# Performance work log

Hardware: AMD Instinct MI355X
Metric: run time of the kernel (lower is better)

Reference implementation:

```python
import jax, jax.numpy as jnp
import numpy as np

N, F, H, C, E = 100000, 128, 128, 40, 1600000


def setup_inputs() -> dict:
    key = jax.random.key(0)
    ks = jax.random.split(key, 8)
    x = jax.random.normal(ks[0], (N, F), dtype=jnp.float32)
    edge_index = jax.random.randint(ks[1], (2, E), 0, N, dtype=jnp.int64)
    s = 0.05
    return {
        "x": x,
        "edge_index": edge_index,
        "eps1": jnp.float32(0.0),
        "w1": jax.random.normal(ks[2], (F, H), dtype=jnp.float32) * s,
        "b1": jnp.zeros((H,), jnp.float32),
        "w2": jax.random.normal(ks[3], (H, H), dtype=jnp.float32) * s,
        "b2": jnp.zeros((H,), jnp.float32),
        "eps2": jnp.float32(0.0),
        "w3": jax.random.normal(ks[4], (H, H), dtype=jnp.float32) * s,
        "b3": jnp.zeros((H,), jnp.float32),
        "w4": jax.random.normal(ks[5], (H, C), dtype=jnp.float32) * s,
        "b4": jnp.zeros((C,), jnp.float32),
    }


def _gin_aggregate(h, src, dst, eps, n):
    # sum_{j -> i} h_j  +  (1+eps) * h_i
    agg = jax.ops.segment_sum(h[src], dst, num_segments=n)
    return (1.0 + eps) * h + agg


def reference(x, edge_index, eps1, w1, b1, w2, b2, eps2, w3, b3, w4, b4):
    src, dst = edge_index[0], edge_index[1]
    n = x.shape[0]
    # conv1: GINConv with MLP = Lin-ReLU-Lin-ReLU
    h = _gin_aggregate(x, src, dst, eps1, n)
    h = jax.nn.relu(h @ w1 + b1)
    h = jax.nn.relu(h @ w2 + b2)
    h = jax.nn.relu(h)  # outer F.relu (idempotent, kept for faithfulness)
    # dropout: identity in eval mode
    # conv2: GINConv with MLP = Lin-ReLU-Lin
    h2 = _gin_aggregate(h, src, dst, eps2, n)
    h2 = jax.nn.relu(h2 @ w3 + b3)
    h2 = h2 @ w4 + b4
    return jax.nn.log_softmax(h2, axis=1)
```

## Files before the change

kernel.cpp:

```cpp
#include <hip/hip_runtime.h>
#include <hip/hip_fp16.h>
#include <math.h>

constexpr int F = 128;
constexpr int C = 40;
constexpr int LDH = 136;
constexpr int BSHIFT = 8;
constexpr int BSIZE = 1 << BSHIFT;
constexpr int CHUNK = 8192;

typedef __attribute__((ext_vector_type(8))) _Float16 half8;
typedef __attribute__((ext_vector_type(4))) float float4v;


__global__ __launch_bounds__(256) void coarse_hist_kernel(const int* __restrict__ dst, int E, int NB,
                                                          int* __restrict__ coarse_count) {
    __shared__ int hist[512];
    int t = threadIdx.x;
    int c0 = blockIdx.x * CHUNK;
    int cend = min(c0 + CHUNK, E);
    for (int i = t; i < NB; i += 256) hist[i] = 0;
    __syncthreads();
    for (int i = c0 + t; i < cend; i += 256)
        atomicAdd(&hist[dst[i] >> BSHIFT], 1);
    __syncthreads();
    for (int i = t; i < NB; i += 256)
        if (hist[i]) atomicAdd(&coarse_count[i], hist[i]);
}

__global__ __launch_bounds__(512) void coarse_scan_kernel(const int* __restrict__ coarse_count,
                                                          int NB, int E,
                                                          int* __restrict__ coarse_start,
                                                          int* __restrict__ bucket_pos,
                                                          int* __restrict__ row_start, int N) {
    __shared__ int tmp[512];
    int t = threadIdx.x;
    int v = (t < NB) ? coarse_count[t] : 0;
    tmp[t] = v;
    __syncthreads();
    for (int d = 1; d < 512; d <<= 1) {
        int add = (t >= d) ? tmp[t - d] : 0;
        __syncthreads();
        tmp[t] += add;
        __syncthreads();
    }
    if (t < NB) {
        int ex = tmp[t] - v;
        coarse_start[t] = ex;
        bucket_pos[t] = ex;
    }
    if (t == 0) {
        coarse_start[NB] = E;
        row_start[N] = E;
    }
}

__global__ __launch_bounds__(256) void bucket_scatter_a_kernel(
        const int* __restrict__ src, const int* __restrict__ dst, int E, int NB,
        int* __restrict__ bucket_pos, unsigned* __restrict__ pairs) {
    __shared__ int hist[512];
    __shared__ int base[512];
    int t = threadIdx.x;
    int c0 = blockIdx.x * CHUNK;
    int cend = min(c0 + CHUNK, E);
    for (int i = t; i < NB; i += 256) hist[i] = 0;
    __syncthreads();
    for (int i = c0 + t; i < cend; i += 256)
        atomicAdd(&hist[dst[i] >> BSHIFT], 1);
    __syncthreads();
    for (int i = t; i < NB; i += 256) {
        int h = hist[i];
        base[i] = (h > 0) ? atomicAdd(&bucket_pos[i], h) : 0;
        hist[i] = 0;
    }
    __syncthreads();
    for (int i = c0 + t; i < cend; i += 256) {
        int d = dst[i];
        int b = d >> BSHIFT;
        int p = base[b] + atomicAdd(&hist[b], 1);
        pairs[p] = ((unsigned)(d & (BSIZE - 1)) << 24) | (unsigned)src[i];
    }
}

__global__ __launch_bounds__(256) void bucket_sort_kernel(const unsigned* __restrict__ pairs,
                                                          const int* __restrict__ coarse_start,
                                                          int N, int* __restrict__ row_start,
                                                          int* __restrict__ src_sorted) {
    __shared__ int hist[256];
    __shared__ int tmp[256];
    int b = blockIdx.x, t = threadIdx.x;
    int base = b << BSHIFT;
    int start = coarse_start[b];
    int end = coarse_start[b + 1];
    hist[t] = 0;
    __syncthreads();
    for (int i = start + t; i < end; i += 256)
        atomicAdd(&hist[pairs[i] >> 24], 1);
    __syncthreads();
    int v = hist[t];
    tmp[t] = v;
    __syncthreads();
    for (int d = 1; d < 256; d <<= 1) {
        int add = (t >= d) ? tmp[t - d] : 0;
        __syncthreads();
        tmp[t] += add;
        __syncthreads();
    }
    int ex = start + tmp[t] - v;
    if (base + t < N) row_start[base + t] = ex;
    hist[t] = ex;
    __syncthreads();
    for (int i = start + t; i < end; i += 256) {
        unsigned u = pairs[i];
        int p = atomicAdd(&hist[u >> 24], 1);
        src_sorted[p] = (int)(u & 0x00FFFFFFu);
    }
}


__global__ void conv_f16_kernel(const float* __restrict__ in, __half* __restrict__ out, int n4,
                                int* __restrict__ coarse_count, int NB) {
    int i = blockIdx.x * blockDim.x + threadIdx.x;
    if (blockIdx.x == 0) {
        for (int j = threadIdx.x; j < NB; j += 256) coarse_count[j] = 0;
    }
    if (i >= n4) return;
    float4 v = ((const float4*)in)[i];
    __half2 a = __floats2half2_rn(v.x, v.y);
    __half2 b = __floats2half2_rn(v.z, v.w);
    uint2 o;
    o.x = __builtin_bit_cast(unsigned, a);
    o.y = __builtin_bit_cast(unsigned, b);
    ((uint2*)out)[i] = o;
}


__global__ __launch_bounds__(256) void prep_weights_kernel(
        const float* __restrict__ w1, const float* __restrict__ w2,
        const float* __restrict__ w3, const float* __restrict__ w4,
        __half* __restrict__ w1t, __half* __restrict__ w2t,
        __half* __restrict__ w3t, __half* __restrict__ w4t) {
    __shared__ float lds[128 * 128];
    const float* in; __half* outp; int Nin, Npad;
    switch (blockIdx.x) {
        case 0:  in = w1; outp = w1t; Nin = 128; Npad = 128; break;
        case 1:  in = w2; outp = w2t; Nin = 128; Npad = 128; break;
        case 2:  in = w3; outp = w3t; Nin = 128; Npad = 128; break;
        default: in = w4; outp = w4t; Nin = 40;  Npad = 48;  break;
    }
    int t = threadIdx.x;
    int nf4 = 128 * Nin / 4;
    for (int i = t; i < nf4; i += 256)
        ((float4*)lds)[i] = ((const float4*)in)[i];
    __syncthreads();
    int total = Npad * 64;
    for (int i = t; i < total; i += 256) {
        int n = i >> 6, k2 = (i & 63) * 2;
        float lo = 0.f, hi = 0.f;
        if (n < Nin) {
            lo = lds[k2 * Nin + n];
            hi = lds[(k2 + 1) * Nin + n];
        }
        __half2 h = __floats2half2_rn(lo, hi);
        ((unsigned*)outp)[i] = __builtin_bit_cast(unsigned, h);
    }
}


__global__ __launch_bounds__(256) void agg_f16_kernel(const __half* __restrict__ feat,
        const int* __restrict__ row_start, const int* __restrict__ src_sorted,
        const float* __restrict__ eps_ptr, __half* __restrict__ out, int N) {
    int wid = (int)((blockIdx.x * blockDim.x + threadIdx.x) >> 6);
    int lane = threadIdx.x & 63;
    if (wid >= N) return;
    int q = lane >> 4, l16 = lane & 15;
    int s = row_start[wid], e = row_start[wid + 1];
    uint4 selfu = *(((const uint4*)(feat + (size_t)wid * F)) + l16);
    float ep1 = 1.0f + *eps_ptr;
    __half2 A0, A1, A2, A3, B0, B1, B2, B3;
    A0 = A1 = A2 = A3 = B0 = B1 = B2 = B3 = __builtin_bit_cast(__half2, 0u);
    const uint4 z4 = make_uint4(0u, 0u, 0u, 0u);
    for (int i0 = s; i0 < e; i0 += 16) {
        int li = i0 + l16;
        int sv = src_sorted[li < e ? li : (e - 1)];
        int s0 = __shfl(sv, q);
        int s1 = __shfl(sv, q + 4);
        int s2 = __shfl(sv, q + 8);
        int s3 = __shfl(sv, q + 12);
        uint4 u0 = *(((const uint4*)(feat + (size_t)s0 * F)) + l16);
        uint4 u1 = *(((const uint4*)(feat + (size_t)s1 * F)) + l16);
        uint4 u2 = *(((const uint4*)(feat + (size_t)s2 * F)) + l16);
        uint4 u3 = *(((const uint4*)(feat + (size_t)s3 * F)) + l16);
        if (i0 + q >= e)      u0 = z4;
        if (i0 + q + 4 >= e)  u1 = z4;
        if (i0 + q + 8 >= e)  u2 = z4;
        if (i0 + q + 12 >= e) u3 = z4;
        A0 = __hadd2(A0, __builtin_bit_cast(__half2, u0.x));
        A1 = __hadd2(A1, __builtin_bit_cast(__half2, u0.y));
        A2 = __hadd2(A2, __builtin_bit_cast(__half2, u0.z));
        A3 = __hadd2(A3, __builtin_bit_cast(__half2, u0.w));
        B0 = __hadd2(B0, __builtin_bit_cast(__half2, u1.x));
        B1 = __hadd2(B1, __builtin_bit_cast(__half2, u1.y));
        B2 = __hadd2(B2, __builtin_bit_cast(__half2, u1.z));
        B3 = __hadd2(B3, __builtin_bit_cast(__half2, u1.w));
        A0 = __hadd2(A0, __builtin_bit_cast(__half2, u2.x));
        A1 = __hadd2(A1, __builtin_bit_cast(__half2, u2.y));
        A2 = __hadd2(A2, __builtin_bit_cast(__half2, u2.z));
        A3 = __hadd2(A3, __builtin_bit_cast(__half2, u2.w));
        B0 = __hadd2(B0, __builtin_bit_cast(__half2, u3.x));
        B1 = __hadd2(B1, __builtin_bit_cast(__half2, u3.y));
        B2 = __hadd2(B2, __builtin_bit_cast(__half2, u3.z));
        B3 = __hadd2(B3, __builtin_bit_cast(__half2, u3.w));
    }
    float a[8];
    {
        float2 fa, fb;
        fa = __half22float2(A0); fb = __half22float2(B0); a[0] = fa.x + fb.x; a[1] = fa.y + fb.y;
        fa = __half22float2(A1); fb = __half22float2(B1); a[2] = fa.x + fb.x; a[3] = fa.y + fb.y;
        fa = __half22float2(A2); fb = __half22float2(B2); a[4] = fa.x + fb.x; a[5] = fa.y + fb.y;
        fa = __half22float2(A3); fb = __half22float2(B3); a[6] = fa.x + fb.x; a[7] = fa.y + fb.y;
    }
#pragma unroll
    for (int j = 0; j < 8; ++j) {
        a[j] += __shfl_xor(a[j], 16);
        a[j] += __shfl_xor(a[j], 32);
    }
    if (q == 0) {
        float2 s0 = __half22float2(__builtin_bit_cast(__half2, selfu.x));
        float2 s1 = __half22float2(__builtin_bit_cast(__half2, selfu.y));
        float2 s2 = __half22float2(__builtin_bit_cast(__half2, selfu.z));
        float2 s3 = __half22float2(__builtin_bit_cast(__half2, selfu.w));
        a[0] = fmaf(ep1, s0.x, a[0]); a[1] = fmaf(ep1, s0.y, a[1]);
        a[2] = fmaf(ep1, s1.x, a[2]); a[3] = fmaf(ep1, s1.y, a[3]);
        a[4] = fmaf(ep1, s2.x, a[4]); a[5] = fmaf(ep1, s2.y, a[5]);
        a[6] = fmaf(ep1, s3.x, a[6]); a[7] = fmaf(ep1, s3.y, a[7]);
        uint4 ou;
        ou.x = __builtin_bit_cast(unsigned, __floats2half2_rn(a[0], a[1]));
        ou.y = __builtin_bit_cast(unsigned, __floats2half2_rn(a[2], a[3]));
        ou.z = __builtin_bit_cast(unsigned, __floats2half2_rn(a[4], a[5]));
        ou.w = __builtin_bit_cast(unsigned, __floats2half2_rn(a[6], a[7]));
        *(((uint4*)(out + (size_t)wid * F)) + l16) = ou;
    }
}


__global__ __launch_bounds__(256) void mlp1_mfma_kernel(const __half* __restrict__ A,
        const __half* __restrict__ w1t, const float* __restrict__ b1,
        const __half* __restrict__ w2t, const float* __restrict__ b2,
        __half* __restrict__ out, int N) {
    __shared__ __half ldsA[64 * LDH];
    __shared__ __half ldsW[128 * LDH];
    __shared__ float ldsB[256];
    int t = threadIdx.x;
    int wave = t >> 6, lane = t & 63, quad = lane >> 4, l16 = lane & 15;
    int br = blockIdx.x * 64;
    if (t < 128) ldsB[t] = b1[t];
    else         ldsB[t] = b2[t - 128];
    for (int i = t; i < 1024; i += 256) {
        int r = i >> 4, c = i & 15;
        int gr = br + r;
        uint4 v = make_uint4(0u, 0u, 0u, 0u);
        if (gr < N) v = *((const uint4*)(A + (size_t)gr * F + c * 8));
        *((uint4*)&ldsA[r * LDH + c * 8]) = v;
    }
    for (int i = t; i < 2048; i += 256) {
        int r = i >> 4, c = i & 15;
        *((uint4*)&ldsW[r * LDH + c * 8]) = *((const uint4*)(w1t + r * 128 + c * 8));
    }
    __syncthreads();

    int ct0 = wave * 2;
    float4v acc[4][2];
    float4v zero = {0.f, 0.f, 0.f, 0.f};
#pragma unroll
    for (int i = 0; i < 4; ++i)
#pragma unroll
        for (int j = 0; j < 2; ++j) acc[i][j] = zero;

#pragma unroll
    for (int ks = 0; ks < 4; ++ks) {
        half8 af[4], wf[2];
#pragma unroll
        for (int i = 0; i < 4; ++i)
            af[i] = *((const half8*)&ldsA[(i * 16 + l16) * LDH + ks * 32 + quad * 8]);
#pragma unroll
        for (int j = 0; j < 2; ++j)
            wf[j] = *((const half8*)&ldsW[((ct0 + j) * 16 + l16) * LDH + ks * 32 + quad * 8]);
#pragma unroll
        for (int i = 0; i < 4; ++i)
#pragma unroll
            for (int j = 0; j < 2; ++j)
                acc[i][j] = __builtin_amdgcn_mfma_f32_16x16x32_f16(wf[j], af[i], acc[i][j], 0, 0, 0);
    }
    __syncthreads();
#pragma unroll
    for (int j = 0; j < 2; ++j) {
        int c = ct0 + j;
        float4 bb = *((const float4*)&ldsB[c * 16 + quad * 4]);
#pragma unroll
        for (int i = 0; i < 4; ++i) {
            float v0 = acc[i][j][0] + bb.x; v0 = v0 > 0.f ? v0 : 0.f;
            float v1 = acc[i][j][1] + bb.y; v1 = v1 > 0.f ? v1 : 0.f;
            float v2 = acc[i][j][2] + bb.z; v2 = v2 > 0.f ? v2 : 0.f;
            float v3 = acc[i][j][3] + bb.w; v3 = v3 > 0.f ? v3 : 0.f;
            __half2 h0 = __floats2half2_rn(v0, v1);
            __half2 h1 = __floats2half2_rn(v2, v3);
            uint2 o;
            o.x = __builtin_bit_cast(unsigned, h0);
            o.y = __builtin_bit_cast(unsigned, h1);
            *((uint2*)&ldsA[(i * 16 + l16) * LDH + c * 16 + quad * 4]) = o;
        }
    }
    for (int i = t; i < 2048; i += 256) {
        int r = i >> 4, c = i & 15;
        *((uint4*)&ldsW[r * LDH + c * 8]) = *((const uint4*)(w2t + r * 128 + c * 8));
    }
    __syncthreads();

#pragma unroll
    for (int i = 0; i < 4; ++i)
#pragma unroll
        for (int j = 0; j < 2; ++j) acc[i][j] = zero;
#pragma unroll
    for (int ks = 0; ks < 4; ++ks) {
        half8 af[4], wf[2];
#pragma unroll
        for (int i = 0; i < 4; ++i)
            af[i] = *((const half8*)&ldsA[(i * 16 + l16) * LDH + ks * 32 + quad * 8]);
#pragma unroll
        for (int j = 0; j < 2; ++j)
            wf[j] = *((const half8*)&ldsW[((ct0 + j) * 16 + l16) * LDH + ks * 32 + quad * 8]);
#pragma unroll
        for (int i = 0; i < 4; ++i)
#pragma unroll
            for (int j = 0; j < 2; ++j)
                acc[i][j] = __builtin_amdgcn_mfma_f32_16x16x32_f16(wf[j], af[i], acc[i][j], 0, 0, 0);
    }
    __syncthreads();
#pragma unroll
    for (int j = 0; j < 2; ++j) {
        int c = ct0 + j;
        float4 bb = *((const float4*)&ldsB[128 + c * 16 + quad * 4]);
#pragma unroll
        for (int i = 0; i < 4; ++i) {
            float v0 = acc[i][j][0] + bb.x; v0 = v0 > 0.f ? v0 : 0.f;
            float v1 = acc[i][j][1] + bb.y; v1 = v1 > 0.f ? v1 : 0.f;
            float v2 = acc[i][j][2] + bb.z; v2 = v2 > 0.f ? v2 : 0.f;
            float v3 = acc[i][j][3] + bb.w; v3 = v3 > 0.f ? v3 : 0.f;
            __half2 h0 = __floats2half2_rn(v0, v1);
            __half2 h1 = __floats2half2_rn(v2, v3);
            uint2 o;
            o.x = __builtin_bit_cast(unsigned, h0);
            o.y = __builtin_bit_cast(unsigned, h1);
            *((uint2*)&ldsA[(i * 16 + l16) * LDH + c * 16 + quad * 4]) = o;
        }
    }
    __syncthreads();
    for (int i = t; i < 1024; i += 256) {
        int r = i >> 4, c = i & 15;
        int gr = br + r;
        if (gr < N)
            *((uint4*)(out + (size_t)gr * F + c * 8)) = *((const uint4*)&ldsA[r * LDH + c * 8]);
    }
}


__global__ __launch_bounds__(256) void mlp2_mfma_kernel(const __half* __restrict__ A,
        const __half* __restrict__ w3t, const float* __restrict__ b3,
        const __half* __restrict__ w4t, const float* __restrict__ b4,
        float* __restrict__ out, int N) {
    __shared__ __half ldsA[64 * LDH];
    __shared__ __half ldsW[128 * LDH];
    __shared__ float ldsB[176];
    int t = threadIdx.x;
    int wave = t >> 6, lane = t & 63, quad = lane >> 4, l16 = lane & 15;
    int br = blockIdx.x * 64;
    if (t < 128) ldsB[t] = b3[t];
    else if (t < 176) ldsB[t] = (t - 128 < C) ? b4[t - 128] : 0.f;
    for (int i = t; i < 1024; i += 256) {
        int r = i >> 4, c = i & 15;
        int gr = br + r;
        uint4 v = make_uint4(0u, 0u, 0u, 0u);
        if (gr < N) v = *((const uint4*)(A + (size_t)gr * F + c * 8));
        *((uint4*)&ldsA[r * LDH + c * 8]) = v;
    }
    for (int i = t; i < 2048; i += 256) {
        int r = i >> 4, c = i & 15;
        *((uint4*)&ldsW[r * LDH + c * 8]) = *((const uint4*)(w3t + r * 128 + c * 8));
    }
    __syncthreads();

    int ct0 = wave * 2;
    float4v acc[4][2];
    float4v zero = {0.f, 0.f, 0.f, 0.f};
#pragma unroll
    for (int i = 0; i < 4; ++i)
#pragma unroll
        for (int j = 0; j < 2; ++j) acc[i][j] = zero;
#pragma unroll
    for (int ks = 0; ks < 4; ++ks) {
        half8 af[4], wf[2];
#pragma unroll
        for (int i = 0; i < 4; ++i)
            af[i] = *((const half8*)&ldsA[(i * 16 + l16) * LDH + ks * 32 + quad * 8]);
#pragma unroll
        for (int j = 0; j < 2; ++j)
            wf[j] = *((const half8*)&ldsW[((ct0 + j) * 16 + l16) * LDH + ks * 32 + quad * 8]);
#pragma unroll
        for (int i = 0; i < 4; ++i)
#pragma unroll
            for (int j = 0; j < 2; ++j)
                acc[i][j] = __builtin_amdgcn_mfma_f32_16x16x32_f16(wf[j], af[i], acc[i][j], 0, 0, 0);
    }
    __syncthreads();
#pragma unroll
    for (int j = 0; j < 2; ++j) {
        int c = ct0 + j;
        float4 bb = *((const float4*)&ldsB[c * 16 + quad * 4]);
#pragma unroll
        for (int i = 0; i < 4; ++i) {
            float v0 = acc[i][j][0] + bb.x; v0 = v0 > 0.f ? v0 : 0.f;
            float v1 = acc[i][j][1] + bb.y; v1 = v1 > 0.f ? v1 : 0.f;
            float v2 = acc[i][j][2] + bb.z; v2 = v2 > 0.f ? v2 : 0.f;
            float v3 = acc[i][j][3] + bb.w; v3 = v3 > 0.f ? v3 : 0.f;
            __half2 h0 = __floats2half2_rn(v0, v1);
            __half2 h1 = __floats2half2_rn(v2, v3);
            uint2 o;
            o.x = __builtin_bit_cast(unsigned, h0);
            o.y = __builtin_bit_cast(unsigned, h1);
            *((uint2*)&ldsA[(i * 16 + l16) * LDH + c * 16 + quad * 4]) = o;
        }
    }
    for (int i = t; i < 768; i += 256) {
        int r = i >> 4, c = i & 15;
        *((uint4*)&ldsW[r * LDH + c * 8]) = *((const uint4*)(w4t + r * 128 + c * 8));
    }
    __syncthreads();

    float4v acc4[3];
#pragma unroll
    for (int c = 0; c < 3; ++c) acc4[c] = zero;
#pragma unroll
    for (int ks = 0; ks < 4; ++ks) {
        half8 af = *((const half8*)&ldsA[(wave * 16 + l16) * LDH + ks * 32 + quad * 8]);
#pragma unroll
        for (int c = 0; c < 3; ++c) {
            half8 wf = *((const half8*)&ldsW[(c * 16 + l16) * LDH + ks * 32 + quad * 8]);
            acc4[c] = __builtin_amdgcn_mfma_f32_16x16x32_f16(wf, af, acc4[c], 0, 0, 0);
        }
    }
    float lv[3][4];
#pragma unroll
    for (int c = 0; c < 3; ++c) {
        float4 bb = *((const float4*)&ldsB[128 + c * 16 + quad * 4]);
        lv[c][0] = acc4[c][0] + bb.x;
        lv[c][1] = acc4[c][1] + bb.y;
        lv[c][2] = acc4[c][2] + bb.z;
        lv[c][3] = acc4[c][3] + bb.w;
    }
    bool tile2ok = (quad < 2);
    float m = -1e30f;
#pragma unroll
    for (int c = 0; c < 3; ++c) {
        if (c == 2 && !tile2ok) continue;
#pragma unroll
        for (int r = 0; r < 4; ++r) m = fmaxf(m, lv[c][r]);
    }
    m = fmaxf(m, __shfl_xor(m, 16));
    m = fmaxf(m, __shfl_xor(m, 32));
    float ssum = 0.f;
#pragma unroll
    for (int c = 0; c < 3; ++c) {
        if (c == 2 && !tile2ok) continue;
#pragma unroll
        for (int r = 0; r < 4; ++r) ssum += __expf(lv[c][r] - m);
    }
    ssum += __shfl_xor(ssum, 16);
    ssum += __shfl_xor(ssum, 32);
    float L = m + __logf(ssum);
    int node = br + wave * 16 + l16;
    if (node < N) {
#pragma unroll
        for (int c = 0; c < 3; ++c) {
            if (c == 2 && !tile2ok) continue;
            float4 o = make_float4(lv[c][0] - L, lv[c][1] - L, lv[c][2] - L, lv[c][3] - L);
            *((float4*)(out + (size_t)node * C + c * 16 + quad * 4)) = o;
        }
    }
}


extern "C" void kernel_launch(void* const* d_in, const int* in_sizes, int n_in,
                              void* d_out, int out_size, void* d_ws, size_t ws_size,
                              hipStream_t stream) {
    const float* x    = (const float*)d_in[0];
    const int*   ei   = (const int*)d_in[1];
    const float* eps1 = (const float*)d_in[2];
    const float* w1   = (const float*)d_in[3];
    const float* b1   = (const float*)d_in[4];
    const float* w2   = (const float*)d_in[5];
    const float* b2   = (const float*)d_in[6];
    const float* eps2 = (const float*)d_in[7];
    const float* w3   = (const float*)d_in[8];
    const float* b3   = (const float*)d_in[9];
    const float* w4   = (const float*)d_in[10];
    const float* b4   = (const float*)d_in[11];
    float* out = (float*)d_out;

    int N = in_sizes[0] / F;
    int E = in_sizes[1] / 2;
    const int* src = ei;
    const int* dst = ei + E;

    int NB = (N + BSIZE - 1) >> BSHIFT;
    int BA = (E + CHUNK - 1) / CHUNK;

    __half* x_h  = (__half*)d_ws;
    __half* h0_h = x_h + (size_t)N * F;
    __half* h_h  = h0_h + (size_t)N * F;
    __half* w1t  = h_h + (size_t)N * F;
    __half* w2t  = w1t + 128 * 128;
    __half* w3t  = w2t + 128 * 128;
    __half* w4t  = w3t + 128 * 128;
    unsigned* pairs   = (unsigned*)(w4t + 48 * 128);
    int* row_start    = (int*)(pairs + E);
    int* src_sorted   = row_start + (N + 1);
    int* coarse_count = src_sorted + E;
    int* coarse_start = coarse_count + 512;
    int* bucket_pos   = coarse_start + 513;

    int n4 = N * F / 4;
    conv_f16_kernel<<<(n4 + 255) / 256, 256, 0, stream>>>(x, x_h, n4, coarse_count, NB);
    prep_weights_kernel<<<4, 256, 0, stream>>>(w1, w2, w3, w4, w1t, w2t, w3t, w4t);

    coarse_hist_kernel<<<BA, 256, 0, stream>>>(dst, E, NB, coarse_count);
    coarse_scan_kernel<<<1, 512, 0, stream>>>(coarse_count, NB, E, coarse_start, bucket_pos,
                                              row_start, N);
    bucket_scatter_a_kernel<<<BA, 256, 0, stream>>>(src, dst, E, NB, bucket_pos, pairs);
    bucket_sort_kernel<<<NB, 256, 0, stream>>>(pairs, coarse_start, N, row_start, src_sorted);

    agg_f16_kernel<<<(N + 3) / 4, 256, 0, stream>>>(x_h, row_start, src_sorted, eps1, h0_h, N);
    mlp1_mfma_kernel<<<(N + 63) / 64, 256, 0, stream>>>(h0_h, w1t, b1, w2t, b2, h_h, N);
    agg_f16_kernel<<<(N + 3) / 4, 256, 0, stream>>>(h_h, row_start, src_sorted, eps2, h0_h, N);
    mlp2_mfma_kernel<<<(N + 63) / 64, 256, 0, stream>>>(h0_h, w3t, b3, w4t, b4, out, N);
}
```

Measured before the change: 346.0 us.

## Fuse neighbor aggregation into MFMA MLP kernels and merge prep kernels

Neighbor aggregation is fused into each MLP kernel: every wave aggregates 16 rows straight into LDS, then the MFMA layers run on that tile, so the intermediate aggregated feature buffer is never written to or read from global memory. Weight fragments are now read directly from global memory (cached) instead of being staged in LDS, which shrinks LDS use. The histogram, weight transpose and x conversion are merged into one launch, with a memset replacing the in-kernel zeroing. The trade-off is less aggregation parallelism per block (64 rows handled serially by 4 waves) and more repeated global weight loads.

```diff
diff --git a/kernel.cpp b/kernel.cpp
--- a/kernel.cpp
+++ b/kernel.cpp
@@ -13,20 +13,64 @@
 typedef __attribute__((ext_vector_type(4))) float float4v;
 
 
-__global__ __launch_bounds__(256) void coarse_hist_kernel(const int* __restrict__ dst, int E, int NB,
-                                                          int* __restrict__ coarse_count) {
-    __shared__ int hist[512];
-    int t = threadIdx.x;
-    int c0 = blockIdx.x * CHUNK;
-    int cend = min(c0 + CHUNK, E);
-    for (int i = t; i < NB; i += 256) hist[i] = 0;
-    __syncthreads();
-    for (int i = c0 + t; i < cend; i += 256)
-        atomicAdd(&hist[dst[i] >> BSHIFT], 1);
-    __syncthreads();
-    for (int i = t; i < NB; i += 256)
-        if (hist[i]) atomicAdd(&coarse_count[i], hist[i]);
-}
+__global__ __launch_bounds__(256) void fused_prep_kernel(
+        const float* __restrict__ x, __half* __restrict__ x_h, int n4,
+        const int* __restrict__ dst, int E, int NB, int* __restrict__ coarse_count,
+        const float* __restrict__ w1, const float* __restrict__ w2,
+        const float* __restrict__ w3, const float* __restrict__ w4,
+        __half* __restrict__ w1t, __half* __restrict__ w2t,
+        __half* __restrict__ w3t, __half* __restrict__ w4t, int BA) {
+    __shared__ float smem[4096];
+    int b = blockIdx.x, t = threadIdx.x;
+    if (b < BA) {
+        int* hist = (int*)smem;
+        int c0 = b * CHUNK, cend = min(c0 + CHUNK, E);
+        for (int i = t; i < NB; i += 256) hist[i] = 0;
+        __syncthreads();
+        for (int i = c0 + t; i < cend; i += 256)
+            atomicAdd(&hist[dst[i] >> BSHIFT], 1);
+        __syncthreads();
+        for (int i = t; i < NB; i += 256)
+            if (hist[i]) atomicAdd(&coarse_count[i], hist[i]);
+        return;
+    }
+    if (b < BA + 4) {
+        const float* in; __half* outp; int Nin, Npad;
+        switch (b - BA) {
+            case 0:  in = w1; outp = w1t; Nin = 128; Npad = 128; break;
+            case 1:  in = w2; outp = w2t; Nin = 128; Npad = 128; break;
+            case 2:  in = w3; outp = w3t; Nin = 128; Npad = 128; break;
+            default: in = w4; outp = w4t; Nin = 40;  Npad = 48;  break;
+        }
+        for (int p = 0; p < 4; ++p) {
+            int nf4 = 32 * Nin / 4;
+            const float4* srcv = (const float4*)(in + 32 * p * Nin);
+            for (int i = t; i < nf4; i += 256) ((float4*)smem)[i] = srcv[i];
+            __syncthreads();
+            int total = Npad * 16;
+            for (int i = t; i < total; i += 256) {
+                int n = i >> 4, wl = i & 15;
+                float lo = 0.f, hi = 0.f;
+                if (n < Nin) {
+                    lo = smem[(2 * wl) * Nin + n];
+                    hi = smem[(2 * wl + 1) * Nin + n];
+                }
+                __half2 h = __floats2half2_rn(lo, hi);
+                ((unsigned*)outp)[n * 64 + 16 * p + wl] = __builtin_bit_cast(unsigned, h);
+            }
+            __syncthreads();
+        }
+        return;
+    }
+    int i = (b - BA - 4) * 256 + t;
+    if (i >= n4) return;
+    float4 v = ((const float4*)x)[i];
+    uint2 o;
+    o.x = __builtin_bit_cast(unsigned, __floats2half2_rn(v.x, v.y));
+    o.y = __builtin_bit_cast(unsigned, __floats2half2_rn(v.z, v.w));
+    ((uint2*)x_h)[i] = o;
+}
+
 
 __global__ __launch_bounds__(512) void coarse_scan_kernel(const int* __restrict__ coarse_count,
                                                           int NB, int E,
@@ -118,154 +162,94 @@
 }
 
 
-__global__ void conv_f16_kernel(const float* __restrict__ in, __half* __restrict__ out, int n4,
-                                int* __restrict__ coarse_count, int NB) {
-    int i = blockIdx.x * blockDim.x + threadIdx.x;
-    if (blockIdx.x == 0) {
-        for (int j = threadIdx.x; j < NB; j += 256) coarse_count[j] = 0;
-    }
-    if (i >= n4) return;
-    float4 v = ((const float4*)in)[i];
-    __half2 a = __floats2half2_rn(v.x, v.y);
-    __half2 b = __floats2half2_rn(v.z, v.w);
-    uint2 o;
-    o.x = __builtin_bit_cast(unsigned, a);
-    o.y = __builtin_bit_cast(unsigned, b);
-    ((uint2*)out)[i] = o;
-}
-
-
-__global__ __launch_bounds__(256) void prep_weights_kernel(
-        const float* __restrict__ w1, const float* __restrict__ w2,
-        const float* __restrict__ w3, const float* __restrict__ w4,
-        __half* __restrict__ w1t, __half* __restrict__ w2t,
-        __half* __restrict__ w3t, __half* __restrict__ w4t) {
-    __shared__ float lds[128 * 128];
-    const float* in; __half* outp; int Nin, Npad;
-    switch (blockIdx.x) {
-        case 0:  in = w1; outp = w1t; Nin = 128; Npad = 128; break;
-        case 1:  in = w2; outp = w2t; Nin = 128; Npad = 128; break;
-        case 2:  in = w3; outp = w3t; Nin = 128; Npad = 128; break;
-        default: in = w4; outp = w4t; Nin = 40;  Npad = 48;  break;
-    }
-    int t = threadIdx.x;
-    int nf4 = 128 * Nin / 4;
-    for (int i = t; i < nf4; i += 256)
-        ((float4*)lds)[i] = ((const float4*)in)[i];
-    __syncthreads();
-    int total = Npad * 64;
-    for (int i = t; i < total; i += 256) {
-        int n = i >> 6, k2 = (i & 63) * 2;
-        float lo = 0.f, hi = 0.f;
-        if (n < Nin) {
-            lo = lds[k2 * Nin + n];
-            hi = lds[(k2 + 1) * Nin + n];
-        }
-        __half2 h = __floats2half2_rn(lo, hi);
-        ((unsigned*)outp)[i] = __builtin_bit_cast(unsigned, h);
-    }
-}
-
-
-__global__ __launch_bounds__(256) void agg_f16_kernel(const __half* __restrict__ feat,
+__global__ __launch_bounds__(256) void gin1_kernel(const __half* __restrict__ feat,
         const int* __restrict__ row_start, const int* __restrict__ src_sorted,
-        const float* __restrict__ eps_ptr, __half* __restrict__ out, int N) {
-    int wid = (int)((blockIdx.x * blockDim.x + threadIdx.x) >> 6);
-    int lane = threadIdx.x & 63;
-    if (wid >= N) return;
-    int q = lane >> 4, l16 = lane & 15;
-    int s = row_start[wid], e = row_start[wid + 1];
-    uint4 selfu = *(((const uint4*)(feat + (size_t)wid * F)) + l16);
-    float ep1 = 1.0f + *eps_ptr;
-    __half2 A0, A1, A2, A3, B0, B1, B2, B3;
-    A0 = A1 = A2 = A3 = B0 = B1 = B2 = B3 = __builtin_bit_cast(__half2, 0u);
-    const uint4 z4 = make_uint4(0u, 0u, 0u, 0u);
-    for (int i0 = s; i0 < e; i0 += 16) {
-        int li = i0 + l16;
-        int sv = src_sorted[li < e ? li : (e - 1)];
-        int s0 = __shfl(sv, q);
-        int s1 = __shfl(sv, q + 4);
-        int s2 = __shfl(sv, q + 8);
-        int s3 = __shfl(sv, q + 12);
-        uint4 u0 = *(((const uint4*)(feat + (size_t)s0 * F)) + l16);
-        uint4 u1 = *(((const uint4*)(feat + (size_t)s1 * F)) + l16);
-        uint4 u2 = *(((const uint4*)(feat + (size_t)s2 * F)) + l16);
-        uint4 u3 = *(((const uint4*)(feat + (size_t)s3 * F)) + l16);
-        if (i0 + q >= e)      u0 = z4;
-        if (i0 + q + 4 >= e)  u1 = z4;
-        if (i0 + q + 8 >= e)  u2 = z4;
-        if (i0 + q + 12 >= e) u3 = z4;
-        A0 = __hadd2(A0, __builtin_bit_cast(__half2, u0.x));
-        A1 = __hadd2(A1, __builtin_bit_cast(__half2, u0.y));
-        A2 = __hadd2(A2, __builtin_bit_cast(__half2, u0.z));
-        A3 = __hadd2(A3, __builtin_bit_cast(__half2, u0.w));
-        B0 = __hadd2(B0, __builtin_bit_cast(__half2, u1.x));
-        B1 = __hadd2(B1, __builtin_bit_cast(__half2, u1.y));
-        B2 = __hadd2(B2, __builtin_bit_cast(__half2, u1.z));
-        B3 = __hadd2(B3, __builtin_bit_cast(__half2, u1.w));
-        A0 = __hadd2(A0, __builtin_bit_cast(__half2, u2.x));
-        A1 = __hadd2(A1, __builtin_bit_cast(__half2, u2.y));
-        A2 = __hadd2(A2, __builtin_bit_cast(__half2, u2.z));
-        A3 = __hadd2(A3, __builtin_bit_cast(__half2, u2.w));
-        B0 = __hadd2(B0, __builtin_bit_cast(__half2, u3.x));
-        B1 = __hadd2(B1, __builtin_bit_cast(__half2, u3.y));
-        B2 = __hadd2(B2, __builtin_bit_cast(__half2, u3.z));
-        B3 = __hadd2(B3, __builtin_bit_cast(__half2, u3.w));
-    }
-    float a[8];
-    {
-        float2 fa, fb;
-        fa = __half22float2(A0); fb = __half22float2(B0); a[0] = fa.x + fb.x; a[1] = fa.y + fb.y;
-        fa = __half22float2(A1); fb = __half22float2(B1); a[2] = fa.x + fb.x; a[3] = fa.y + fb.y;
-        fa = __half22float2(A2); fb = __half22float2(B2); a[4] = fa.x + fb.x; a[5] = fa.y + fb.y;
-        fa = __half22float2(A3); fb = __half22float2(B3); a[6] = fa.x + fb.x; a[7] = fa.y + fb.y;
-    }
-#pragma unroll
-    for (int j = 0; j < 8; ++j) {
-        a[j] += __shfl_xor(a[j], 16);
-        a[j] += __shfl_xor(a[j], 32);
-    }
-    if (q == 0) {
-        float2 s0 = __half22float2(__builtin_bit_cast(__half2, selfu.x));
-        float2 s1 = __half22float2(__builtin_bit_cast(__half2, selfu.y));
-        float2 s2 = __half22float2(__builtin_bit_cast(__half2, selfu.z));
-        float2 s3 = __half22float2(__builtin_bit_cast(__half2, selfu.w));
-        a[0] = fmaf(ep1, s0.x, a[0]); a[1] = fmaf(ep1, s0.y, a[1]);
-        a[2] = fmaf(ep1, s1.x, a[2]); a[3] = fmaf(ep1, s1.y, a[3]);
-        a[4] = fmaf(ep1, s2.x, a[4]); a[5] = fmaf(ep1, s2.y, a[5]);
-        a[6] = fmaf(ep1, s3.x, a[6]); a[7] = fmaf(ep1, s3.y, a[7]);
-        uint4 ou;
-        ou.x = __builtin_bit_cast(unsigned, __floats2half2_rn(a[0], a[1]));
-        ou.y = __builtin_bit_cast(unsigned, __floats2half2_rn(a[2], a[3]));
-        ou.z = __builtin_bit_cast(unsigned, __floats2half2_rn(a[4], a[5]));
-        ou.w = __builtin_bit_cast(unsigned, __floats2half2_rn(a[6], a[7]));
-        *(((uint4*)(out + (size_t)wid * F)) + l16) = ou;
-    }
-}
-
-
-__global__ __launch_bounds__(256) void mlp1_mfma_kernel(const __half* __restrict__ A,
+        const float* __restrict__ eps_ptr,
         const __half* __restrict__ w1t, const float* __restrict__ b1,
         const __half* __restrict__ w2t, const float* __restrict__ b2,
         __half* __restrict__ out, int N) {
     __shared__ __half ldsA[64 * LDH];
-    __shared__ __half ldsW[128 * LDH];
     __shared__ float ldsB[256];
     int t = threadIdx.x;
-    int wave = t >> 6, lane = t & 63, quad = lane >> 4, l16 = lane & 15;
+    int wave = t >> 6, lane = t & 63, q = lane >> 4, l16 = lane & 15;
     int br = blockIdx.x * 64;
     if (t < 128) ldsB[t] = b1[t];
     else         ldsB[t] = b2[t - 128];
-    for (int i = t; i < 1024; i += 256) {
-        int r = i >> 4, c = i & 15;
-        int gr = br + r;
-        uint4 v = make_uint4(0u, 0u, 0u, 0u);
-        if (gr < N) v = *((const uint4*)(A + (size_t)gr * F + c * 8));
-        *((uint4*)&ldsA[r * LDH + c * 8]) = v;
-    }
-    for (int i = t; i < 2048; i += 256) {
-        int r = i >> 4, c = i & 15;
-        *((uint4*)&ldsW[r * LDH + c * 8]) = *((const uint4*)(w1t + r * 128 + c * 8));
+    float ep1 = 1.0f + *eps_ptr;
+    const uint4 z4 = make_uint4(0u, 0u, 0u, 0u);
+
+    for (int k = 0; k < 16; ++k) {
+        int rrow = wave * 16 + k;
+        int n = br + rrow;
+        if (n < N) {
+            int s = row_start[n], e = row_start[n + 1];
+            uint4 selfu = *(((const uint4*)(feat + (size_t)n * F)) + l16);
+            __half2 A0, A1, A2, A3, B0, B1, B2, B3;
+            A0 = A1 = A2 = A3 = B0 = B1 = B2 = B3 = __builtin_bit_cast(__half2, 0u);
+            for (int i0 = s; i0 < e; i0 += 16) {
+                int li = i0 + l16;
+                int sv = src_sorted[li < e ? li : (e - 1)];
+                int s0 = __shfl(sv, q);
+                int s1 = __shfl(sv, q + 4);
+                int s2 = __shfl(sv, q + 8);
+                int s3 = __shfl(sv, q + 12);
+                uint4 u0 = *(((const uint4*)(feat + (size_t)s0 * F)) + l16);
+                uint4 u1 = *(((const uint4*)(feat + (size_t)s1 * F)) + l16);
+                uint4 u2 = *(((const uint4*)(feat + (size_t)s2 * F)) + l16);
+                uint4 u3 = *(((const uint4*)(feat + (size_t)s3 * F)) + l16);
+                if (i0 + q >= e)      u0 = z4;
+                if (i0 + q + 4 >= e)  u1 = z4;
+                if (i0 + q + 8 >= e)  u2 = z4;
+                if (i0 + q + 12 >= e) u3 = z4;
+                A0 = __hadd2(A0, __builtin_bit_cast(__half2, u0.x));
+                A1 = __hadd2(A1, __builtin_bit_cast(__half2, u0.y));
+                A2 = __hadd2(A2, __builtin_bit_cast(__half2, u0.z));
+                A3 = __hadd2(A3, __builtin_bit_cast(__half2, u0.w));
+                B0 = __hadd2(B0, __builtin_bit_cast(__half2, u1.x));
+                B1 = __hadd2(B1, __builtin_bit_cast(__half2, u1.y));
+                B2 = __hadd2(B2, __builtin_bit_cast(__half2, u1.z));
+                B3 = __hadd2(B3, __builtin_bit_cast(__half2, u1.w));
+                A0 = __hadd2(A0, __builtin_bit_cast(__half2, u2.x));
+                A1 = __hadd2(A1, __builtin_bit_cast(__half2, u2.y));
+                A2 = __hadd2(A2, __builtin_bit_cast(__half2, u2.z));
+                A3 = __hadd2(A3, __builtin_bit_cast(__half2, u2.w));
+                B0 = __hadd2(B0, __builtin_bit_cast(__half2, u3.x));
+                B1 = __hadd2(B1, __builtin_bit_cast(__half2, u3.y));
+                B2 = __hadd2(B2, __builtin_bit_cast(__half2, u3.z));
+                B3 = __hadd2(B3, __builtin_bit_cast(__half2, u3.w));
+            }
+            float a[8];
+            {
+                float2 fa, fb;
+                fa = __half22float2(A0); fb = __half22float2(B0); a[0] = fa.x + fb.x; a[1] = fa.y + fb.y;
+                fa = __half22float2(A1); fb = __half22float2(B1); a[2] = fa.x + fb.x; a[3] = fa.y + fb.y;
+                fa = __half22float2(A2); fb = __half22float2(B2); a[4] = fa.x + fb.x; a[5] = fa.y + fb.y;
+                fa = __half22float2(A3); fb = __half22float2(B3); a[6] = fa.x + fb.x; a[7] = fa.y + fb.y;
+            }
+#pragma unroll
+            for (int j = 0; j < 8; ++j) {
+                a[j] += __shfl_xor(a[j], 16);
+                a[j] += __shfl_xor(a[j], 32);
+            }
+            if (q == 0) {
+                float2 s0 = __half22float2(__builtin_bit_cast(__half2, selfu.x));
+                float2 s1 = __half22float2(__builtin_bit_cast(__half2, selfu.y));
+                float2 s2 = __half22float2(__builtin_bit_cast(__half2, selfu.z));
+                float2 s3 = __half22float2(__builtin_bit_cast(__half2, selfu.w));
+                a[0] = fmaf(ep1, s0.x, a[0]); a[1] = fmaf(ep1, s0.y, a[1]);
+                a[2] = fmaf(ep1, s1.x, a[2]); a[3] = fmaf(ep1, s1.y, a[3]);
+                a[4] = fmaf(ep1, s2.x, a[4]); a[5] = fmaf(ep1, s2.y, a[5]);
+                a[6] = fmaf(ep1, s3.x, a[6]); a[7] = fmaf(ep1, s3.y, a[7]);
+                uint4 ou;
+                ou.x = __builtin_bit_cast(unsigned, __floats2half2_rn(a[0], a[1]));
+                ou.y = __builtin_bit_cast(unsigned, __floats2half2_rn(a[2], a[3]));
+                ou.z = __builtin_bit_cast(unsigned, __floats2half2_rn(a[4], a[5]));
+                ou.w = __builtin_bit_cast(unsigned, __floats2half2_rn(a[6], a[7]));
+                *((uint4*)&ldsA[rrow * LDH + l16 * 8]) = ou;
+            }
+        } else if (q == 0) {
+            *((uint4*)&ldsA[rrow * LDH + l16 * 8]) = z4;
+        }
     }
     __syncthreads();
 
@@ -276,16 +260,15 @@
     for (int i = 0; i < 4; ++i)
 #pragma unroll
         for (int j = 0; j < 2; ++j) acc[i][j] = zero;
-
 #pragma unroll
     for (int ks = 0; ks < 4; ++ks) {
         half8 af[4], wf[2];
 #pragma unroll
         for (int i = 0; i < 4; ++i)
-            af[i] = *((const half8*)&ldsA[(i * 16 + l16) * LDH + ks * 32 + quad * 8]);
+            af[i] = *((const half8*)&ldsA[(i * 16 + l16) * LDH + ks * 32 + q * 8]);
 #pragma unroll
         for (int j = 0; j < 2; ++j)
-            wf[j] = *((const half8*)&ldsW[((ct0 + j) * 16 + l16) * LDH + ks * 32 + quad * 8]);
+            wf[j] = *((const half8*)(w1t + ((ct0 + j) * 16 + l16) * 128 + ks * 32 + q * 8));
 #pragma unroll
         for (int i = 0; i < 4; ++i)
 #pragma unroll
@@ -296,27 +279,20 @@
 #pragma unroll
     for (int j = 0; j < 2; ++j) {
         int c = ct0 + j;
-        float4 bb = *((const float4*)&ldsB[c * 16 + quad * 4]);
+        float4 bb = *((const float4*)&ldsB[c * 16 + q * 4]);
 #pragma unroll
         for (int i = 0; i < 4; ++i) {
             float v0 = acc[i][j][0] + bb.x; v0 = v0 > 0.f ? v0 : 0.f;
             float v1 = acc[i][j][1] + bb.y; v1 = v1 > 0.f ? v1 : 0.f;
             float v2 = acc[i][j][2] + bb.z; v2 = v2 > 0.f ? v2 : 0.f;
             float v3 = acc[i][j][3] + bb.w; v3 = v3 > 0.f ? v3 : 0.f;
-            __half2 h0 = __floats2half2_rn(v0, v1);
-            __half2 h1 = __floats2half2_rn(v2, v3);
             uint2 o;
-            o.x = __builtin_bit_cast(unsigned, h0);
-            o.y = __builtin_bit_cast(unsigned, h1);
-            *((uint2*)&ldsA[(i * 16 + l16) * LDH + c * 16 + quad * 4]) = o;
-        }
-    }
-    for (int i = t; i < 2048; i += 256) {
-        int r = i >> 4, c = i & 15;
-        *((uint4*)&ldsW[r * LDH + c * 8]) = *((const uint4*)(w2t + r * 128 + c * 8));
-    }
-    __syncthreads();
-
+            o.x = __builtin_bit_cast(unsigned, __floats2half2_rn(v0, v1));
+            o.y = __builtin_bit_cast(unsigned, __floats2half2_rn(v2, v3));
+            *((uint2*)&ldsA[(i * 16 + l16) * LDH + c * 16 + q * 4]) = o;
+        }
+    }
+    __syncthreads();
 #pragma unroll
     for (int i = 0; i < 4; ++i)
 #pragma unroll
@@ -326,10 +302,10 @@
         half8 af[4], wf[2];
 #pragma unroll
         for (int i = 0; i < 4; ++i)
-            af[i] = *((const half8*)&ldsA[(i * 16 + l16) * LDH + ks * 32 + quad * 8]);
+            af[i] = *((const half8*)&ldsA[(i * 16 + l16) * LDH + ks * 32 + q * 8]);
 #pragma unroll
         for (int j = 0; j < 2; ++j)
-            wf[j] = *((const half8*)&ldsW[((ct0 + j) * 16 + l16) * LDH + ks * 32 + quad * 8]);
+            wf[j] = *((const half8*)(w2t + ((ct0 + j) * 16 + l16) * 128 + ks * 32 + q * 8));
 #pragma unroll
         for (int i = 0; i < 4; ++i)
 #pragma unroll
@@ -340,19 +316,17 @@
 #pragma unroll
     for (int j = 0; j < 2; ++j) {
         int c = ct0 + j;
-        float4 bb = *((const float4*)&ldsB[128 + c * 16 + quad * 4]);
+        float4 bb = *((const float4*)&ldsB[128 + c * 16 + q * 4]);
 #pragma unroll
         for (int i = 0; i < 4; ++i) {
             float v0 = acc[i][j][0] + bb.x; v0 = v0 > 0.f ? v0 : 0.f;
             float v1 = acc[i][j][1] + bb.y; v1 = v1 > 0.f ? v1 : 0.f;
             float v2 = acc[i][j][2] + bb.z; v2 = v2 > 0.f ? v2 : 0.f;
             float v3 = acc[i][j][3] + bb.w; v3 = v3 > 0.f ? v3 : 0.f;
-            __half2 h0 = __floats2half2_rn(v0, v1);
-            __half2 h1 = __floats2half2_rn(v2, v3);
             uint2 o;
-            o.x = __builtin_bit_cast(unsigned, h0);
-            o.y = __builtin_bit_cast(unsigned, h1);
-            *((uint2*)&ldsA[(i * 16 + l16) * LDH + c * 16 + quad * 4]) = o;
+            o.x = __builtin_bit_cast(unsigned, __floats2half2_rn(v0, v1));
+            o.y = __builtin_bit_cast(unsigned, __floats2half2_rn(v2, v3));
+            *((uint2*)&ldsA[(i * 16 + l16) * LDH + c * 16 + q * 4]) = o;
         }
     }
     __syncthreads();
@@ -365,28 +339,94 @@
 }
 
 
-__global__ __launch_bounds__(256) void mlp2_mfma_kernel(const __half* __restrict__ A,
+__global__ __launch_bounds__(256) void gin2_kernel(const __half* __restrict__ feat,
+        const int* __restrict__ row_start, const int* __restrict__ src_sorted,
+        const float* __restrict__ eps_ptr,
         const __half* __restrict__ w3t, const float* __restrict__ b3,
         const __half* __restrict__ w4t, const float* __restrict__ b4,
         float* __restrict__ out, int N) {
     __shared__ __half ldsA[64 * LDH];
-    __shared__ __half ldsW[128 * LDH];
     __shared__ float ldsB[176];
     int t = threadIdx.x;
-    int wave = t >> 6, lane = t & 63, quad = lane >> 4, l16 = lane & 15;
+    int wave = t >> 6, lane = t & 63, q = lane >> 4, l16 = lane & 15;
     int br = blockIdx.x * 64;
     if (t < 128) ldsB[t] = b3[t];
     else if (t < 176) ldsB[t] = (t - 128 < C) ? b4[t - 128] : 0.f;
-    for (int i = t; i < 1024; i += 256) {
-        int r = i >> 4, c = i & 15;
-        int gr = br + r;
-        uint4 v = make_uint4(0u, 0u, 0u, 0u);
-        if (gr < N) v = *((const uint4*)(A + (size_t)gr * F + c * 8));
-        *((uint4*)&ldsA[r * LDH + c * 8]) = v;
-    }
-    for (int i = t; i < 2048; i += 256) {
-        int r = i >> 4, c = i & 15;
-        *((uint4*)&ldsW[r * LDH + c * 8]) = *((const uint4*)(w3t + r * 128 + c * 8));
+    float ep1 = 1.0f + *eps_ptr;
+    const uint4 z4 = make_uint4(0u, 0u, 0u, 0u);
+
+    for (int k = 0; k < 16; ++k) {
+        int rrow = wave * 16 + k;
+        int n = br + rrow;
+        if (n < N) {
+            int s = row_start[n], e = row_start[n + 1];
+            uint4 selfu = *(((const uint4*)(feat + (size_t)n * F)) + l16);
+            __half2 A0, A1, A2, A3, B0, B1, B2, B3;
+            A0 = A1 = A2 = A3 = B0 = B1 = B2 = B3 = __builtin_bit_cast(__half2, 0u);
+            for (int i0 = s; i0 < e; i0 += 16) {
+                int li = i0 + l16;
+                int sv = src_sorted[li < e ? li : (e - 1)];
+                int s0 = __shfl(sv, q);
+                int s1 = __shfl(sv, q + 4);
+                int s2 = __shfl(sv, q + 8);
+                int s3 = __shfl(sv, q + 12);
+                uint4 u0 = *(((const uint4*)(feat + (size_t)s0 * F)) + l16);
+                uint4 u1 = *(((const uint4*)(feat + (size_t)s1 * F)) + l16);
+                uint4 u2 = *(((const uint4*)(feat + (size_t)s2 * F)) + l16);
+                uint4 u3 = *(((const uint4*)(feat + (size_t)s3 * F)) + l16);
+                if (i0 + q >= e)      u0 = z4;
+                if (i0 + q + 4 >= e)  u1 = z4;
+                if (i0 + q + 8 >= e)  u2 = z4;
+                if (i0 + q + 12 >= e) u3 = z4;
+                A0 = __hadd2(A0, __builtin_bit_cast(__half2, u0.x));
+                A1 = __hadd2(A1, __builtin_bit_cast(__half2, u0.y));
+                A2 = __hadd2(A2, __builtin_bit_cast(__half2, u0.z));
+                A3 = __hadd2(A3, __builtin_bit_cast(__half2, u0.w));
+                B0 = __hadd2(B0, __builtin_bit_cast(__half2, u1.x));
+                B1 = __hadd2(B1, __builtin_bit_cast(__half2, u1.y));
+                B2 = __hadd2(B2, __builtin_bit_cast(__half2, u1.z));
+                B3 = __hadd2(B3, __builtin_bit_cast(__half2, u1.w));
+                A0 = __hadd2(A0, __builtin_bit_cast(__half2, u2.x));
+                A1 = __hadd2(A1, __builtin_bit_cast(__half2, u2.y));
+                A2 = __hadd2(A2, __builtin_bit_cast(__half2, u2.z));
+                A3 = __hadd2(A3, __builtin_bit_cast(__half2, u2.w));
+                B0 = __hadd2(B0, __builtin_bit_cast(__half2, u3.x));
+                B1 = __hadd2(B1, __builtin_bit_cast(__half2, u3.y));
+                B2 = __hadd2(B2, __builtin_bit_cast(__half2, u3.z));
+                B3 = __hadd2(B3, __builtin_bit_cast(__half2, u3.w));
+            }
+            float a[8];
+            {
+                float2 fa, fb;
+                fa = __half22float2(A0); fb = __half22float2(B0); a[0] = fa.x + fb.x; a[1] = fa.y + fb.y;
+                fa = __half22float2(A1); fb = __half22float2(B1); a[2] = fa.x + fb.x; a[3] = fa.y + fb.y;
+                fa = __half22float2(A2); fb = __half22float2(B2); a[4] = fa.x + fb.x; a[5] = fa.y + fb.y;
+                fa = __half22float2(A3); fb = __half22float2(B3); a[6] = fa.x + fb.x; a[7] = fa.y + fb.y;
+            }
+#pragma unroll
+            for (int j = 0; j < 8; ++j) {
+                a[j] += __shfl_xor(a[j], 16);
+                a[j] += __shfl_xor(a[j], 32);
+            }
+            if (q == 0) {
+                float2 s0 = __half22float2(__builtin_bit_cast(__half2, selfu.x));
+                float2 s1 = __half22float2(__builtin_bit_cast(__half2, selfu.y));
+                float2 s2 = __half22float2(__builtin_bit_cast(__half2, selfu.z));
+                float2 s3 = __half22float2(__builtin_bit_cast(__half2, selfu.w));
+                a[0] = fmaf(ep1, s0.x, a[0]); a[1] = fmaf(ep1, s0.y, a[1]);
+                a[2] = fmaf(ep1, s1.x, a[2]); a[3] = fmaf(ep1, s1.y, a[3]);
+                a[4] = fmaf(ep1, s2.x, a[4]); a[5] = fmaf(ep1, s2.y, a[5]);
+                a[6] = fmaf(ep1, s3.x, a[6]); a[7] = fmaf(ep1, s3.y, a[7]);
+                uint4 ou;
+                ou.x = __builtin_bit_cast(unsigned, __floats2half2_rn(a[0], a[1]));
+                ou.y = __builtin_bit_cast(unsigned, __floats2half2_rn(a[2], a[3]));
+                ou.z = __builtin_bit_cast(unsigned, __floats2half2_rn(a[4], a[5]));
+                ou.w = __builtin_bit_cast(unsigned, __floats2half2_rn(a[6], a[7]));
+                *((uint4*)&ldsA[rrow * LDH + l16 * 8]) = ou;
+            }
+        } else if (q == 0) {
+            *((uint4*)&ldsA[rrow * LDH + l16 * 8]) = z4;
+        }
     }
     __syncthreads();
 
@@ -402,10 +442,10 @@
         half8 af[4], wf[2];
 #pragma unroll
         for (int i = 0; i < 4; ++i)
-            af[i] = *((const half8*)&ldsA[(i * 16 + l16) * LDH + ks * 32 + quad * 8]);
+            af[i] = *((const half8*)&ldsA[(i * 16 + l16) * LDH + ks * 32 + q * 8]);
 #pragma unroll
         for (int j = 0; j < 2; ++j)
-            wf[j] = *((const half8*)&ldsW[((ct0 + j) * 16 + l16) * LDH + ks * 32 + quad * 8]);
+            wf[j] = *((const half8*)(w3t + ((ct0 + j) * 16 + l16) * 128 + ks * 32 + q * 8));
 #pragma unroll
         for (int i = 0; i < 4; ++i)
 #pragma unroll
@@ -416,24 +456,18 @@
 #pragma unroll
     for (int j = 0; j < 2; ++j) {
         int c = ct0 + j;
-        float4 bb = *((const float4*)&ldsB[c * 16 + quad * 4]);
+        float4 bb = *((const float4*)&ldsB[c * 16 + q * 4]);
 #pragma unroll
         for (int i = 0; i < 4; ++i) {
             float v0 = acc[i][j][0] + bb.x; v0 = v0 > 0.f ? v0 : 0.f;
             float v1 = acc[i][j][1] + bb.y; v1 = v1 > 0.f ? v1 : 0.f;
             float v2 = acc[i][j][2] + bb.z; v2 = v2 > 0.f ? v2 : 0.f;
             float v3 = acc[i][j][3] + bb.w; v3 = v3 > 0.f ? v3 : 0.f;
-            __half2 h0 = __floats2half2_rn(v0, v1);
-            __half2 h1 = __floats2half2_rn(v2, v3);
             uint2 o;
-            o.x = __builtin_bit_cast(unsigned, h0);
-            o.y = __builtin_bit_cast(unsigned, h1);
-            *((uint2*)&ldsA[(i * 16 + l16) * LDH + c * 16 + quad * 4]) = o;
-        }
-    }
-    for (int i = t; i < 768; i += 256) {
-        int r = i >> 4, c = i & 15;
-        *((uint4*)&ldsW[r * LDH + c * 8]) = *((const uint4*)(w4t + r * 128 + c * 8));
+            o.x = __builtin_bit_cast(unsigned, __floats2half2_rn(v0, v1));
+            o.y = __builtin_bit_cast(unsigned, __floats2half2_rn(v2, v3));
+            *((uint2*)&ldsA[(i * 16 + l16) * LDH + c * 16 + q * 4]) = o;
+        }
     }
     __syncthreads();
 
@@ -442,23 +476,23 @@
     for (int c = 0; c < 3; ++c) acc4[c] = zero;
 #pragma unroll
     for (int ks = 0; ks < 4; ++ks) {
-        half8 af = *((const half8*)&ldsA[(wave * 16 + l16) * LDH + ks * 32 + quad * 8]);
+        half8 af = *((const half8*)&ldsA[(wave * 16 + l16) * LDH + ks * 32 + q * 8]);
 #pragma unroll
         for (int c = 0; c < 3; ++c) {
-            half8 wf = *((const half8*)&ldsW[(c * 16 + l16) * LDH + ks * 32 + quad * 8]);
+            half8 wf = *((const half8*)(w4t + (c * 16 + l16) * 128 + ks * 32 + q * 8));
             acc4[c] = __builtin_amdgcn_mfma_f32_16x16x32_f16(wf, af, acc4[c], 0, 0, 0);
         }
     }
     float lv[3][4];
 #pragma unroll
     for (int c = 0; c < 3; ++c) {
-        float4 bb = *((const float4*)&ldsB[128 + c * 16 + quad * 4]);
+        float4 bb = *((const float4*)&ldsB[128 + c * 16 + q * 4]);
         lv[c][0] = acc4[c][0] + bb.x;
         lv[c][1] = acc4[c][1] + bb.y;
         lv[c][2] = acc4[c][2] + bb.z;
         lv[c][3] = acc4[c][3] + bb.w;
     }
-    bool tile2ok = (quad < 2);
+    bool tile2ok = (q < 2);
     float m = -1e30f;
 #pragma unroll
     for (int c = 0; c < 3; ++c) {
@@ -484,7 +518,7 @@
         for (int c = 0; c < 3; ++c) {
             if (c == 2 && !tile2ok) continue;
             float4 o = make_float4(lv[c][0] - L, lv[c][1] - L, lv[c][2] - L, lv[c][3] - L);
-            *((float4*)(out + (size_t)node * C + c * 16 + quad * 4)) = o;
+            *((float4*)(out + (size_t)node * C + c * 16 + q * 4)) = o;
         }
     }
 }
@@ -516,8 +550,7 @@
     int BA = (E + CHUNK - 1) / CHUNK;
 
     __half* x_h  = (__half*)d_ws;
-    __half* h0_h = x_h + (size_t)N * F;
-    __half* h_h  = h0_h + (size_t)N * F;
+    __half* h_h  = x_h + (size_t)N * F;
     __half* w1t  = h_h + (size_t)N * F;
     __half* w2t  = w1t + 128 * 128;
     __half* w3t  = w2t + 128 * 128;
@@ -530,17 +563,20 @@
     int* bucket_pos   = coarse_start + 513;
 
     int n4 = N * F / 4;
-    conv_f16_kernel<<<(n4 + 255) / 256, 256, 0, stream>>>(x, x_h, n4, coarse_count, NB);
-    prep_weights_kernel<<<4, 256, 0, stream>>>(w1, w2, w3, w4, w1t, w2t, w3t, w4t);
-
-    coarse_hist_kernel<<<BA, 256, 0, stream>>>(dst, E, NB, coarse_count);
+    int NCONV = (n4 + 255) / 256;
+
+    hipMemsetAsync(coarse_count, 0, 512 * sizeof(int), stream);
+    fused_prep_kernel<<<BA + 4 + NCONV, 256, 0, stream>>>(x, x_h, n4, dst, E, NB, coarse_count,
+                                                          w1, w2, w3, w4, w1t, w2t, w3t, w4t, BA);
+
     coarse_scan_kernel<<<1, 512, 0, stream>>>(coarse_count, NB, E, coarse_start, bucket_pos,
                                               row_start, N);
     bucket_scatter_a_kernel<<<BA, 256, 0, stream>>>(src, dst, E, NB, bucket_pos, pairs);
     bucket_sort_kernel<<<NB, 256, 0, stream>>>(pairs, coarse_start, N, row_start, src_sorted);
 
-    agg_f16_kernel<<<(N + 3) / 4, 256, 0, stream>>>(x_h, row_start, src_sorted, eps1, h0_h, N);
-    mlp1_mfma_kernel<<<(N + 63) / 64, 256, 0, stream>>>(h0_h, w1t, b1, w2t, b2, h_h, N);
-    agg_f16_kernel<<<(N + 3) / 4, 256, 0, stream>>>(h_h, row_start, src_sorted, eps2, h0_h, N);
-    mlp2_mfma_kernel<<<(N + 63) / 64, 256, 0, stream>>>(h0_h, w3t, b3, w4t, b4, out, N);
-}
+    int nblk = (N + 63) / 64;
+    gin1_kernel<<<nblk, 256, 0, stream>>>(x_h, row_start, src_sorted, eps1, w1t, b1, w2t, b2,
+                                          h_h, N);
+    gin2_kernel<<<nblk, 256, 0, stream>>>(h_h, row_start, src_sorted, eps2, w3t, b3, w4t, b4,
+                                          out, N);
+}
```

Result: slower. 358.0 us (+3.5%).
